# Kernel optimization log

Hardware: AMD Instinct MI355X
Metric: run time of the kernel (lower is better)

The kernel has to match this reference:

```python
import jax, jax.numpy as jnp
import numpy as np

K = 4          # neighbors
R = 2          # step_ratio
O = 64         # output_size


def setup_inputs() -> dict:
    key = jax.random.key(0)
    ks = jax.random.split(key, 7)
    B, C, N = 16, 128, 2048
    x = jax.random.normal(ks[0], (B, C, N), jnp.float32)
    # 1x1 conv weights stored as [out, in]; bias [out]
    w1 = jax.random.normal(ks[1], (O, 2 * C), jnp.float32) * (1.0 / np.sqrt(2 * C))
    b1 = jax.random.normal(ks[2], (O,), jnp.float32) * 0.01
    w2 = jax.random.normal(ks[3], (O * R, 2 * C + O), jnp.float32) * (1.0 / np.sqrt(2 * C + O))
    b2 = jax.random.normal(ks[4], (O * R,), jnp.float32) * 0.01
    w3 = jax.random.normal(ks[5], (O, O), jnp.float32) * (1.0 / np.sqrt(O))
    b3 = jax.random.normal(ks[6], (O,), jnp.float32) * 0.01
    return {"x": x, "w1": w1, "b1": b1, "w2": w2, "b2": b2, "w3": w3, "b3": b3}


def _knn_idx(x, k):
    # x: [B, C, N]; returns indices of k nearest neighbors (incl. self) [B, N, k]
    inner = -2.0 * jnp.einsum('bcn,bcm->bnm', x, x)           # [B, N, N]
    xx = jnp.sum(x * x, axis=1)                                # [B, N]
    pd = -xx[:, :, None] - inner - xx[:, None, :]              # negative sq dist
    return jax.lax.top_k(pd, k)[1]                             # [B, N, k]


def _graph_feature(x, k):
    # minus_center=False variant used by EF_expansion
    idx = _knn_idx(x, k)                                       # [B, N, k]
    xt = jnp.transpose(x, (0, 2, 1))                           # [B, N, C]
    feat = jax.vmap(lambda xb, ib: xb[ib])(xt, idx)            # [B, N, k, C]
    center = jnp.broadcast_to(xt[:, :, None, :], feat.shape)   # [B, N, k, C]
    f = jnp.concatenate([center, feat], axis=3)                # [B, N, k, 2C]
    return jnp.transpose(f, (0, 3, 1, 2))                      # [B, 2C, N, k]


def _conv1x1(w, b, x):
    # x: [B, Cin, H, W] -> [B, Cout, H, W]
    return jnp.einsum('oc,bchw->bohw', w, x) + b[None, :, None, None]


def reference(x, w1, b1, w2, b2, w3, b3):
    B, C, N = x.shape
    ief = jnp.transpose(_graph_feature(x, K), (0, 1, 3, 2))    # [B, 2C, k, N]
    e1 = _conv1x1(w1, b1, ief)                                 # [B, O, k, N]
    e = jax.nn.relu(jnp.concatenate([e1, ief], axis=1))        # [B, O+2C, k, N]
    e2 = jax.nn.relu(_conv1x1(w2, b2, e))                      # [B, O*R, k, N]
    # [B,O*R,k,N] -> [B,k,N,O*R] -> [B,k,N*R,O] -> [B,O,k,N*R]
    e2 = jnp.transpose(e2, (0, 2, 3, 1)).reshape(B, K, N * R, O)
    e2 = jnp.transpose(e2, (0, 3, 1, 2))
    e3 = _conv1x1(w3, b3, e2)                                  # [B, O, k, N*R]
    return jnp.max(e3, axis=2)                                 # [B, O, N*R]
```

## Files before the change

### kernel.cpp

```cpp
#include <hip/hip_runtime.h>
#include <cstdint>
#include <cstddef>

#define B_  16
#define C_  128
#define N_  2048
#define K_  4
#define O_  64
#define C2_ 256
#define ED_ 320
#define NM_ 4096
#define ROWB 256
#define AGC 384

typedef float  f32x4  __attribute__((ext_vector_type(4)));
typedef short  s16x8  __attribute__((ext_vector_type(8)));
typedef __bf16 bf16x4 __attribute__((ext_vector_type(4)));
typedef __bf16 bf16x8 __attribute__((ext_vector_type(8)));
typedef unsigned short u16;
typedef unsigned int   u32;
typedef unsigned int   u32x4 __attribute__((ext_vector_type(4)));

__device__ __forceinline__ u32 umin32(u32 a, u32 b) { return a < b ? a : b; }
__device__ __forceinline__ u32 umax32(u32 a, u32 b) { return a > b ? a : b; }
__device__ __forceinline__ float bf2f(u16 h) { return __builtin_bit_cast(float, (u32)h << 16); }

__device__ __forceinline__ s16x8 ldw_bf16(const float* __restrict__ p) {
  float4 a = *(const float4*)p;
  float4 c = *(const float4*)(p + 4);
  bf16x8 r;
  r[0] = (__bf16)a.x; r[1] = (__bf16)a.y; r[2] = (__bf16)a.z; r[3] = (__bf16)a.w;
  r[4] = (__bf16)c.x; r[5] = (__bf16)c.y; r[6] = (__bf16)c.z; r[7] = (__bf16)c.w;
  return __builtin_bit_cast(s16x8, r);
}

__device__ __forceinline__ u32 relu2(u32 u) {
  u32 s = u & 0x80008000u;
  u32 m = s - (s >> 15);
  return u & ~(m | s);
}
__device__ __forceinline__ s16x8 relu8(s16x8 v) {
  u32x4 u = __builtin_bit_cast(u32x4, v);
  u[0] = relu2(u[0]); u[1] = relu2(u[1]);
  u[2] = relu2(u[2]); u[3] = relu2(u[3]);
  return __builtin_bit_cast(s16x8, u);
}

__device__ __forceinline__ void glds16(const void* g, void* l) {
  __builtin_amdgcn_global_load_lds(
      (const __attribute__((address_space(1))) u32*)g,
      (__attribute__((address_space(3))) u32*)l, 16, 0, 0);
}

__global__ __launch_bounds__(256) void prep_kernel(const float* __restrict__ x,
                                                   const float* __restrict__ w1,
                                                   const float* __restrict__ w2,
                                                   const float* __restrict__ w3,
                                                   float* __restrict__ xT32,
                                                   u16* __restrict__ xh,
                                                   float* __restrict__ xx,
                                                   u16* __restrict__ wh,
                                                   u16* __restrict__ wg) {
  const int t = threadIdx.x;
  if (blockIdx.y == B_) {
    const int gid = blockIdx.x * 256 + t;
    for (int i = gid; i < 15360; i += 8192) {
      const float* src; u16* dst;
      if (i < 4096)       { src = w1 + (size_t)i * 4;            dst = wh + (size_t)i * 4; }
      else if (i < 14336) { src = w2 + (size_t)(i - 4096) * 4;   dst = wh + 16384 + (size_t)(i - 4096) * 4; }
      else                { src = w3 + (size_t)(i - 14336) * 4;  dst = wh + 57344 + (size_t)(i - 14336) * 4; }
      float4 v = *(const float4*)src;
      ushort4 h;
      h.x = __builtin_bit_cast(u16, (__bf16)v.x);
      h.y = __builtin_bit_cast(u16, (__bf16)v.y);
      h.z = __builtin_bit_cast(u16, (__bf16)v.z);
      h.w = __builtin_bit_cast(u16, (__bf16)v.w);
      *(ushort4*)dst = h;
    }
    if (wg) {
      for (int i = gid; i < 12288; i += 8192) {
        int r = i >> 5;
        int c4 = (i & 31) * 4;
        const float* src;
        if (r < 64)       src = w1 + (size_t)r * C2_ + c4;
        else if (r < 128) src = w1 + (size_t)(r - 64) * C2_ + 128 + c4;
        else if (r < 256) src = w2 + (size_t)(r - 128) * ED_ + 64 + c4;
        else              src = w2 + (size_t)(r - 256) * ED_ + 192 + c4;
        float4 v = *(const float4*)src;
        ushort4 h;
        h.x = __builtin_bit_cast(u16, (__bf16)v.x);
        h.y = __builtin_bit_cast(u16, (__bf16)v.y);
        h.z = __builtin_bit_cast(u16, (__bf16)v.z);
        h.w = __builtin_bit_cast(u16, (__bf16)v.w);
        *(ushort4*)&wg[(size_t)r * 128 + c4] = h;
      }
    }
    return;
  }

  __shared__ __align__(16) float sx[C_][65];
  const int b = blockIdx.y, n0 = blockIdx.x * 64;
  const float* xb = x + (size_t)b * C_ * N_;
  for (int u = t; u < C_ * 16; u += 256) {
    int c = u >> 4, f4 = u & 15;
    float4 v = *(const float4*)&xb[(size_t)c * N_ + n0 + f4 * 4];
    sx[c][f4 * 4 + 0] = v.x; sx[c][f4 * 4 + 1] = v.y;
    sx[c][f4 * 4 + 2] = v.z; sx[c][f4 * 4 + 3] = v.w;
  }
  __syncthreads();
  if (t < 64) {
    float s = 0.f;
    for (int c = 0; c < C_; ++c) { float v = sx[c][t]; s = fmaf(v, v, s); }
    xx[b * N_ + n0 + t] = s;
  }
  for (int u = t; u < 64 * 16; u += 256) {
    int n = u >> 4, cb = u & 15;
    float vv[8]; s16x8 hv;
#pragma unroll
    for (int j = 0; j < 8; ++j) {
      float v = sx[cb * 8 + j][n];
      vv[j] = v;
      hv[j] = (short)__builtin_bit_cast(u16, (__bf16)v);
    }
    size_t ro = ((size_t)b * N_ + n0 + n) * C_;
    *(float4*)&xT32[ro + cb * 8]     = make_float4(vv[0], vv[1], vv[2], vv[3]);
    *(float4*)&xT32[ro + cb * 8 + 4] = make_float4(vv[4], vv[5], vv[6], vv[7]);
    int sc = cb ^ (n & 7);
    *(s16x8*)&xh[ro + sc * 8] = hv;
  }
}

__global__ __launch_bounds__(256) void knn_mfma(const u16* __restrict__ xh,
                                                const float* __restrict__ xx,
                                                int* __restrict__ cand8) {
  __shared__ __align__(16) char smem[40960];
  const int b = blockIdx.y, q0 = blockIdx.x * 64;
  const int t = threadIdx.x;
  const int lane = t & 63, wv = t >> 6, lq = t & 15, lh = (t >> 4) & 3;
  const u16* xhb = xh + (size_t)b * N_ * C_;
  const float* xxb = xx + b * N_;

  s16x8 qf[4][4];
#pragma unroll
  for (int qt = 0; qt < 4; ++qt)
#pragma unroll
    for (int ks = 0; ks < 4; ++ks) {
      int q = q0 + qt * 16 + lq;
      int ch = (ks * 4 + lh) ^ (q & 7);
      qf[qt][ks] = *(const s16x8*)&xhb[(size_t)q * C_ + ch * 8];
    }

  u32 pk[4][5];
#pragma unroll
  for (int qt = 0; qt < 4; ++qt)
#pragma unroll
    for (int s = 0; s < 5; ++s) pk[qt][s] = 0xFFFFFFFFu;

  auto stage = [&](int bufi, int m0) {
    const char* s = (const char*)(xhb + (size_t)m0 * C_);
    char* d = smem + bufi * 16384;
#pragma unroll
    for (int c = 0; c < 4; ++c) {
      int off = (wv * 4 + c) * 1024;
      glds16(s + off + lane * 16, d + off);
    }
  };

  stage(0, 0);
  asm volatile("s_waitcnt vmcnt(0)");
  __syncthreads();

  for (int step = 0; step < 32; ++step) {
    const int cur = step & 1;
    if (step < 31) stage(cur ^ 1, (step + 1) * 64);
    const char* mb = smem + cur * 16384;
    f32x4 acc[4];
#pragma unroll
    for (int qt = 0; qt < 4; ++qt) acc[qt] = (f32x4){0.f, 0.f, 0.f, 0.f};
#pragma unroll
    for (int ks = 0; ks < 4; ++ks) {
      int row = wv * 16 + lq;
      int ch = (ks * 4 + lh) ^ (lq & 7);
      s16x8 mf = *(const s16x8*)(mb + row * 256 + ch * 16);
#pragma unroll
      for (int qt = 0; qt < 4; ++qt)
        acc[qt] = __builtin_amdgcn_mfma_f32_16x16x32_bf16(mf, qf[qt][ks], acc[qt], 0, 0, 0);
    }
    const int mrow = step * 64 + wv * 16 + lh * 4;
    float4 xm4 = *(const float4*)&xxb[mrow];
    float xma[4] = {xm4.x, xm4.y, xm4.z, xm4.w};
#pragma unroll
    for (int r = 0; r < 4; ++r) {
#pragma unroll
      for (int qt = 0; qt < 4; ++qt) {
        float dd = fmaf(acc[qt][r], -2.f, xma[r]);
        u32 s = __builtin_bit_cast(u32, dd);
        u32 neg = (u32)((int)s >> 31);
        u32 u = s ^ (neg | 0x80000000u);
        u32 v = (u & 0xFFFFF800u) | (u32)(mrow + r);
#pragma unroll
        for (int s5 = 0; s5 < 5; ++s5) {
          u32 lo = umin32(v, pk[qt][s5]);
          v = umax32(v, pk[qt][s5]);
          pk[qt][s5] = lo;
        }
      }
    }
    asm volatile("s_waitcnt vmcnt(0)");
    __syncthreads();
  }

  u32* cd = (u32*)smem;
  const int unit = wv * 4 + lh;
#pragma unroll
  for (int qt = 0; qt < 4; ++qt) {
    int ql = qt * 16 + lq;
#pragma unroll
    for (int s = 0; s < 5; ++s) cd[ql * 85 + unit * 5 + s] = pk[qt][s];
  }
  __syncthreads();
  if (t < 64) {
    u32 fd[8];
#pragma unroll
    for (int s = 0; s < 8; ++s) fd[s] = 0xFFFFFFFFu;
    for (int j = 0; j < 80; ++j) {
      u32 v = cd[t * 85 + j];
#pragma unroll
      for (int s = 0; s < 8; ++s) {
        u32 lo = umin32(v, fd[s]);
        v = umax32(v, fd[s]);
        fd[s] = lo;
      }
    }
#pragma unroll
    for (int s = 0; s < 8; ++s)
      cand8[((size_t)b * N_ + q0 + t) * 8 + s] = (int)(fd[s] & 0x7FFu);
  }
}

__global__ __launch_bounds__(256) void rerank_kernel(const float* __restrict__ xT32,
                                                     const float* __restrict__ xx,
                                                     const int* __restrict__ cand8,
                                                     int* __restrict__ knn_out) {
  __shared__ __align__(16) float sq[64][132];
  __shared__ float sd[64][8];
  __shared__ int   si[64][8];
  const int b = blockIdx.y, n0 = blockIdx.x * 64;
  const int t = threadIdx.x;
  const float* xb32 = xT32 + (size_t)b * N_ * C_;
  for (int u = t; u < 64 * 32; u += 256) {
    int n = u >> 5, seg = u & 31;
    *(float4*)&sq[n][seg * 4] = *(const float4*)&xb32[(size_t)(n0 + n) * C_ + seg * 4];
  }
  __syncthreads();
  const int ql = t >> 2, cs = t & 3;
#pragma unroll
  for (int cc = 0; cc < 2; ++cc) {
    int cslot = cs + cc * 4;
    int idx = cand8[((size_t)b * N_ + n0 + ql) * 8 + cslot];
    const float* mr = &xb32[(size_t)idx * C_];
    float a0 = 0.f, a1 = 0.f, a2 = 0.f, a3 = 0.f;
#pragma unroll 8
    for (int i = 0; i < 32; ++i) {
      float4 qv = *(const float4*)&sq[ql][i * 4];
      float4 mv = *(const float4*)&mr[i * 4];
      a0 = fmaf(qv.x, mv.x, a0); a1 = fmaf(qv.y, mv.y, a1);
      a2 = fmaf(qv.z, mv.z, a2); a3 = fmaf(qv.w, mv.w, a3);
    }
    float dot = (a0 + a1) + (a2 + a3);
    sd[ql][cslot] = xx[(size_t)b * N_ + idx] - 2.f * dot;
    si[ql][cslot] = idx;
  }
  __syncthreads();
  if (t < 64) {
    float dloc[8]; int iloc[8];
#pragma unroll
    for (int j = 0; j < 8; ++j) { dloc[j] = sd[t][j]; iloc[j] = si[t][j]; }
    u32 used = 0;
#pragma unroll
    for (int s = 0; s < 4; ++s) {
      float bdv = 1e30f; int bidx = 0x7fffffff; int bj = 0;
#pragma unroll
      for (int j = 0; j < 8; ++j) {
        if (!((used >> j) & 1)) {
          bool bet = (dloc[j] < bdv) || (dloc[j] == bdv && iloc[j] < bidx);
          if (bet) { bdv = dloc[j]; bidx = iloc[j]; bj = j; }
        }
      }
      used |= 1u << bj;
      knn_out[((size_t)b * N_ + n0 + t) * K_ + s] = bidx;
    }
  }
}

__global__ __launch_bounds__(256, 2) void agemm_kernel(
    const u16* __restrict__ xh, const u16* __restrict__ wg,
    const float* __restrict__ b1, const float* __restrict__ b2,
    u16* __restrict__ ag) {
  __shared__ __align__(16) char sm[66560];
  u16* outT = (u16*)(sm + 16384);
  const int b = blockIdx.y, m0 = blockIdx.x * 64;
  const int t = threadIdx.x, lane = t & 63, wv = t >> 6, lq = t & 15, lh = (t >> 4) & 3;
  const u16* xhb = xh + (size_t)b * N_ * C_;

  {
    const char* s = (const char*)(xhb + (size_t)m0 * C_);
#pragma unroll
    for (int c = 0; c < 4; ++c) {
      int off = (wv * 4 + c) * 1024;
      glds16(s + off + lane * 16, sm + off);
    }
  }

  s16x8 af[6][4];
#pragma unroll
  for (int rt = 0; rt < 6; ++rt)
#pragma unroll
    for (int ks = 0; ks < 4; ++ks)
      af[rt][ks] = *(const s16x8*)&wg[(size_t)(wv * 96 + rt * 16 + lq) * 128 + ks * 32 + lh * 8];

  f32x4 acc[6][4];
#pragma unroll
  for (int rt = 0; rt < 6; ++rt)
#pragma unroll
    for (int cg = 0; cg < 4; ++cg) acc[rt][cg] = (f32x4){0.f, 0.f, 0.f, 0.f};

  asm volatile("s_waitcnt vmcnt(0)");
  __syncthreads();

#pragma unroll
  for (int cg = 0; cg < 4; ++cg) {
    s16x8 braw[4], brel[4];
#pragma unroll
    for (int ks = 0; ks < 4; ++ks) {
      int row = cg * 16 + lq;
      braw[ks] = *(const s16x8*)(sm + row * 256 + (((ks * 4 + lh) ^ (lq & 7)) * 16));
      brel[ks] = relu8(braw[ks]);
    }
#pragma unroll
    for (int rt = 0; rt < 6; ++rt) {
      const bool rl = (wv * 96 + rt * 16) >= 128;
#pragma unroll
      for (int ks = 0; ks < 4; ++ks)
        acc[rt][cg] = __builtin_amdgcn_mfma_f32_16x16x32_bf16(
            af[rt][ks], rl ? brel[ks] : braw[ks], acc[rt][cg], 0, 0, 0);
    }
  }

#pragma unroll
  for (int rt = 0; rt < 6; ++rt) {
    const int ch0 = wv * 96 + rt * 16 + lh * 4;
    float bias[4];
#pragma unroll
    for (int r = 0; r < 4; ++r) {
      int c = ch0 + r;
      bias[r] = (c < 64) ? b1[c] : ((c >= 128 && c < 256) ? b2[c - 128] : 0.f);
    }
#pragma unroll
    for (int cg = 0; cg < 4; ++cg) {
      bf16x4 st;
#pragma unroll
      for (int r = 0; r < 4; ++r) st[r] = (__bf16)(acc[rt][cg][r] + bias[r]);
      *(bf16x4*)&outT[(size_t)(cg * 16 + lq) * 392 + ch0] = st;
    }
  }
  __syncthreads();
// ... 55 lines not shown
    for (int q = 0; q < 4; ++q) {
      s16x8 va = *(const s16x8*)&rc[128 + p * 32 + q * 8];
      s16x8 vb = *(const s16x8*)&rn[256 + p * 32 + q * 8];
      bf16x8 r;
#pragma unroll
      for (int j = 0; j < 8; ++j)
        r[j] = (__bf16)(bf2f((u16)va[j]) + bf2f((u16)vb[j]));
      *(bf16x8*)&s2T[(size_t)col * 136 + p * 32 + q * 8] = r;
    }
  }
  __syncthreads();

  {
    f32x4 acc[2][4];
#pragma unroll
    for (int rt = 0; rt < 2; ++rt)
#pragma unroll
      for (int cg = 0; cg < 4; ++cg) acc[rt][cg] = (f32x4){0.f, 0.f, 0.f, 0.f};
#pragma unroll
    for (int ks = 0; ks < 2; ++ks)
#pragma unroll
      for (int cg = 0; cg < 4; ++cg) {
        s16x8 bf = *(const s16x8*)&e1T[(size_t)(cg * 16 + lq) * 72 + ks * 32 + lh * 8];
#pragma unroll
        for (int rt = 0; rt < 2; ++rt)
          acc[rt][cg] = __builtin_amdgcn_mfma_f32_16x16x32_bf16(w2f[rt][ks], bf, acc[rt][cg], 0, 0, 0);
      }
#pragma unroll
    for (int rt = 0; rt < 2; ++rt)
#pragma unroll
      for (int cg = 0; cg < 4; ++cg) {
        const int col = cg * 16 + lq;
        const int j0 = wv * 32 + rt * 16 + lh * 4;
        ushort4 sv = *(const ushort4*)&s2T[(size_t)col * 136 + j0];
        bf16x4 st;
        st[0] = (__bf16)fmaxf(acc[rt][cg][0] + bf2f(sv.x), 0.f);
        st[1] = (__bf16)fmaxf(acc[rt][cg][1] + bf2f(sv.y), 0.f);
        st[2] = (__bf16)fmaxf(acc[rt][cg][2] + bf2f(sv.z), 0.f);
        st[3] = (__bf16)fmaxf(acc[rt][cg][3] + bf2f(sv.w), 0.f);
        *(bf16x4*)&e2T[(size_t)col * 136 + j0] = st;
      }
  }
  __syncthreads();

  {
#pragma unroll
    for (int cg = 0; cg < 8; ++cg) {
      int col = cg * 16 + lq;
      int nl = col >> 3, rr = (col >> 2) & 1, kk = col & 3;
      int row = nl * 4 + kk;
      s16x8 f1 = *(const s16x8*)&e2T[(size_t)row * 136 + rr * 64 + lh * 8];
      s16x8 f2 = *(const s16x8*)&e2T[(size_t)row * 136 + rr * 64 + 32 + lh * 8];
      f32x4 acc = {0.f, 0.f, 0.f, 0.f};
      acc = __builtin_amdgcn_mfma_f32_16x16x32_bf16(w3a, f1, acc, 0, 0, 0);
      acc = __builtin_amdgcn_mfma_f32_16x16x32_bf16(w3b, f2, acc, 0, 0, 0);
      float vv[4];
#pragma unroll
      for (int r = 0; r < 4; ++r) {
        float v = acc[r];
        v = fmaxf(v, __shfl_xor(v, 1));
        v = fmaxf(v, __shfl_xor(v, 2));
        vv[r] = v;
      }
      if ((lq & 3) == 0) {
        int mloc = col >> 2;
        int o = wv * 16 + lh * 4;
        const float b3a[4] = {b3v.x, b3v.y, b3v.z, b3v.w};
#pragma unroll
        for (int r = 0; r < 4; ++r) oSt[(size_t)(o + r) * 36 + mloc] = vv[r] + b3a[r];
      }
    }
  }
  __syncthreads();

#pragma unroll
  for (int io = 0; io < 2; ++io) {
    int u = t + io * 256;
    int o = u >> 3, seg = u & 7;
    *(float4*)&out[((size_t)b * O_ + o) * NM_ + n0 * 2 + seg * 4] =
        *(const float4*)&oSt[(size_t)o * 36 + seg * 4];
  }
}

__global__ __launch_bounds__(256, 2) void fused_tiled(
    const u16* __restrict__ xh, const u16* __restrict__ wh,
    const int* __restrict__ knn_idx,
    const float* __restrict__ b1, const float* __restrict__ b2,
    const float* __restrict__ b3, float* __restrict__ out) {
  __shared__ __align__(16) char fsm[66560];
  __bf16* e1T = (__bf16*)(fsm + 40960);
  float*  oSt = (float*)(fsm + 40960);
  char*   e2T = fsm + 50176;

  const int t  = threadIdx.x;
  const int lane = t & 63, wv = t >> 6, lq = t & 15, lh = (t >> 4) & 3;
  const int b = blockIdx.y;
  const int nbase = blockIdx.x * 64;
  const u16* xhb = xh + (size_t)b * N_ * C_;
  const int kb = (b * N_ + nbase) * K_;

  s16x8 w1f[8], w2f0[10], w2f1[10], w3f[2];
  {
    const u16* r1 = wh + (size_t)(wv * 16 + lq) * C2_;
#pragma unroll
    for (int ks = 0; ks < 8; ++ks) w1f[ks] = *(const s16x8*)&r1[ks * 32 + lh * 8];
    const u16* r20 = wh + 16384 + (size_t)(wv * 32 + lq) * ED_;
    const u16* r21 = r20 + (size_t)16 * ED_;
#pragma unroll
    for (int ks = 0; ks < 10; ++ks) {
      w2f0[ks] = *(const s16x8*)&r20[ks * 32 + lh * 8];
      w2f1[ks] = *(const s16x8*)&r21[ks * 32 + lh * 8];
    }
    const u16* r3 = wh + 57344 + (size_t)(wv * 16 + lq) * O_;
    w3f[0] = *(const s16x8*)&r3[lh * 8];
    w3f[1] = *(const s16x8*)&r3[32 + lh * 8];
  }
  const float4 b1v  = *(const float4*)&b1[wv * 16 + lh * 4];
  const float4 b2v0 = *(const float4*)&b2[wv * 32 + lh * 4];
  const float4 b2v1 = *(const float4*)&b2[wv * 32 + 16 + lh * 4];
  const float4 b3v  = *(const float4*)&b3[wv * 16 + lh * 4];

  auto stageTile = [&](int it, const int* nids) {
    char* cb = fsm + (it & 1) * 20480;
    char* nb = cb + 4096;
    glds16((const char*)xhb + (size_t)(nbase + it * 16 + wv * 4) * ROWB + lane * 16,
           cb + wv * 4 * ROWB);
#pragma unroll
    for (int g = 0; g < 4; ++g) {
      int col = wv * 16 + g * 4 + (lane >> 4);
      int nid = nids[g];
      int sc = (lane & 15) ^ (col & 7) ^ (nid & 7);
      glds16((const char*)xhb + (size_t)nid * ROWB + sc * 16,
             nb + (wv * 16 + g * 4) * ROWB);
    }
  };

  int nids[4];
#pragma unroll
  for (int g = 0; g < 4; ++g)
    nids[g] = knn_idx[kb + wv * 16 + g * 4 + (lane >> 4)];
  stageTile(0, nids);

  for (int it = 0; it < 4; ++it) {
    if (it < 3) {
#pragma unroll
      for (int g = 0; g < 4; ++g)
        nids[g] = knn_idx[kb + (it + 1) * 64 + wv * 16 + g * 4 + (lane >> 4)];
    }
    asm volatile("s_waitcnt vmcnt(0)" ::: "memory");
    __syncthreads();
    if (it < 3) stageTile(it + 1, nids);

    const char* cb = fsm + (it & 1) * 20480;
    const char* nb = cb + 4096;

    {
      f32x4 acc1[4];
#pragma unroll
      for (int cg = 0; cg < 4; ++cg) acc1[cg] = (f32x4){0.f, 0.f, 0.f, 0.f};
#pragma unroll
      for (int ks = 0; ks < 8; ++ks) {
#pragma unroll
        for (int cg = 0; cg < 4; ++cg) {
          const char* bp;
          if (ks < 4) {
            int r = cg * 4 + (lq >> 2);
            bp = cb + r * ROWB + (((ks * 4 + lh) ^ (r & 7)) * 16);
          } else {
            int r = cg * 16 + lq;
            bp = nb + r * ROWB + ((((ks - 4) * 4 + lh) ^ (r & 7)) * 16);
          }
          acc1[cg] = __builtin_amdgcn_mfma_f32_16x16x32_bf16(
              w1f[ks], *(const s16x8*)bp, acc1[cg], 0, 0, 0);
        }
      }
      const float bb[4] = {b1v.x, b1v.y, b1v.z, b1v.w};
#pragma unroll
      for (int cg = 0; cg < 4; ++cg) {
        bf16x4 st;
#pragma unroll
        for (int r = 0; r < 4; ++r) st[r] = (__bf16)fmaxf(acc1[cg][r] + bb[r], 0.f);
        *(bf16x4*)&e1T[(cg * 16 + lq) * 72 + wv * 16 + lh * 4] = st;
      }
    }
    __syncthreads();

    {
      f32x4 acc2[2][4];
#pragma unroll
      for (int ro = 0; ro < 2; ++ro)
#pragma unroll
        for (int cg = 0; cg < 4; ++cg) acc2[ro][cg] = (f32x4){0.f, 0.f, 0.f, 0.f};
#pragma unroll
      for (int ks = 0; ks < 10; ++ks) {
#pragma unroll
        for (int cg = 0; cg < 4; ++cg) {
          s16x8 bf;
          if (ks < 2) {
            bf = *(const s16x8*)&e1T[(cg * 16 + lq) * 72 + ks * 32 + lh * 8];
          } else if (ks < 6) {
            int r = cg * 4 + (lq >> 2);
            bf = relu8(*(const s16x8*)(cb + r * ROWB + ((((ks - 2) * 4 + lh) ^ (r & 7)) * 16)));
          } else {
            int r = cg * 16 + lq;
            bf = relu8(*(const s16x8*)(nb + r * ROWB + ((((ks - 6) * 4 + lh) ^ (r & 7)) * 16)));
          }
          acc2[0][cg] = __builtin_amdgcn_mfma_f32_16x16x32_bf16(w2f0[ks], bf, acc2[0][cg], 0, 0, 0);
          acc2[1][cg] = __builtin_amdgcn_mfma_f32_16x16x32_bf16(w2f1[ks], bf, acc2[1][cg], 0, 0, 0);
        }
      }
      const float c0[4] = {b2v0.x, b2v0.y, b2v0.z, b2v0.w};
      const float c1[4] = {b2v1.x, b2v1.y, b2v1.z, b2v1.w};
#pragma unroll
      for (int ro = 0; ro < 2; ++ro)
#pragma unroll
        for (int cg = 0; cg < 4; ++cg) {
          int col = cg * 16 + lq;
          int e = wv * 32 + ro * 16 + lh * 4;
          int j = e >> 3, sub = e & 7;
          int pos = j ^ (col & 7);
          bf16x4 st;
#pragma unroll
          for (int r = 0; r < 4; ++r) {
            float v = acc2[ro][cg][r] + (ro ? c1[r] : c0[r]);
            st[r] = (__bf16)fmaxf(v, 0.f);
          }
          *(bf16x4*)(e2T + col * ROWB + pos * 16 + sub * 2) = st;
        }
    }
    __syncthreads();

    {
#pragma unroll
      for (int cg = 0; cg < 8; ++cg) {
        int col = cg * 16 + lq;
        int nl = col >> 3, rr = (col >> 2) & 1, kk = col & 3;
        int row = nl * 4 + kk;
        int j1 = rr * 8 + lh, j2 = rr * 8 + 4 + lh;
        s16x8 f1 = *(const s16x8*)(e2T + row * ROWB + ((j1 ^ (row & 7)) * 16));
        s16x8 f2 = *(const s16x8*)(e2T + row * ROWB + ((j2 ^ (row & 7)) * 16));
        f32x4 acc = {0.f, 0.f, 0.f, 0.f};
        acc = __builtin_amdgcn_mfma_f32_16x16x32_bf16(w3f[0], f1, acc, 0, 0, 0);
        acc = __builtin_amdgcn_mfma_f32_16x16x32_bf16(w3f[1], f2, acc, 0, 0, 0);
        float vv[4];
#pragma unroll
        for (int r = 0; r < 4; ++r) {
          float v = acc[r];
          v = fmaxf(v, __shfl_xor(v, 1));
          v = fmaxf(v, __shfl_xor(v, 2));
          vv[r] = v;
        }
        if ((lq & 3) == 0) {
          int mloc = col >> 2;
          int o = wv * 16 + lh * 4;
          const float b3a[4] = {b3v.x, b3v.y, b3v.z, b3v.w};
#pragma unroll
          for (int r = 0; r < 4; ++r) oSt[(o + r) * 36 + mloc] = vv[r] + b3a[r];
        }
      }
    }
    __syncthreads();

#pragma unroll
    for (int io = 0; io < 2; ++io) {
      int u = t + io * 256;
      int o = u >> 3, seg = u & 7;
      *(float4*)&out[((size_t)b * O_ + o) * NM_ + nbase * 2 + it * 32 + seg * 4] =
          *(const float4*)&oSt[o * 36 + seg * 4];
    }
  }
}

__global__ __launch_bounds__(256) void xx_kernel(const float* __restrict__ x,
                                                 float* __restrict__ xx) {
  int g = blockIdx.x * 256 + threadIdx.x;
  int b = g >> 11;
  int n = g & (N_ - 1);
  const float* xp = x + (size_t)b * C_ * N_ + n;
  float s = 0.f;
#pragma unroll 8
  for (int c = 0; c < C_; ++c) { float v = xp[(size_t)c * N_]; s += v * v; }
  xx[g] = s;
}

__global__ __launch_bounds__(256) void knn_kernel(const float* __restrict__ x,
                                                  const float* __restrict__ xx,
                                                  int* __restrict__ knn_out) {
  __shared__ __align__(16) float qT[C_ * 64];
  __shared__ __align__(16) float mT[C_ * 64];
  const int b = blockIdx.y;
  const int q0 = blockIdx.x * 64;
  const int t = threadIdx.x;
  const float* xb = x + (size_t)b * C_ * N_;
  const float* xxb = xx + b * N_;
  for (int i = t; i < C_ * 64; i += 256) {
    int c = i >> 6, q = i & 63;
    qT[i] = xb[(size_t)c * N_ + q0 + q];
  }
  const int tq = t & 15;
  const int tm = t >> 4;
  float bd[4][4]; int bi[4][4];
#pragma unroll
  for (int a = 0; a < 4; ++a)
#pragma unroll
    for (int s = 0; s < 4; ++s) { bd[a][s] = 1e30f; bi[a][s] = 0; }
  for (int m0 = 0; m0 < N_; m0 += 64) {
    __syncthreads();
    for (int i = t; i < C_ * 64; i += 256) {
      int c = i >> 6, m = i & 63;
      mT[i] = xb[(size_t)c * N_ + m0 + m];
    }
    __syncthreads();
    float acc[4][4];
#pragma unroll
    for (int a = 0; a < 4; ++a)
#pragma unroll
      for (int j = 0; j < 4; ++j) acc[a][j] = 0.f;
#pragma unroll 4
    for (int c = 0; c < C_; ++c) {
      float4 qv = *(const float4*)&qT[c * 64 + tq * 4];
      float4 mv = *(const float4*)&mT[c * 64 + tm * 4];
      float qa[4] = {qv.x, qv.y, qv.z, qv.w};
      float ma[4] = {mv.x, mv.y, mv.z, mv.w};
#pragma unroll
      for (int a = 0; a < 4; ++a)
#pragma unroll
        for (int j = 0; j < 4; ++j) acc[a][j] += qa[a] * ma[j];
    }
#pragma unroll
    for (int j = 0; j < 4; ++j) {
      float xm = xxb[m0 + tm * 4 + j];
      int id = m0 + tm * 4 + j;
#pragma unroll
      for (int a = 0; a < 4; ++a) {
        float d = xm - 2.f * acc[a][j];
        if (d < bd[a][3]) {
          bd[a][3] = d; bi[a][3] = id;
#pragma unroll
          for (int s = 3; s > 0; --s)
            if (bd[a][s] < bd[a][s - 1]) {
              float td = bd[a][s]; bd[a][s] = bd[a][s - 1]; bd[a][s - 1] = td;
              int ti = bi[a][s]; bi[a][s] = bi[a][s - 1]; bi[a][s - 1] = ti;
            }
        }
      }
    }
  }
  __syncthreads();
  float* cd = qT;
  int* ci = (int*)mT;
#pragma unroll
  for (int a = 0; a < 4; ++a) {
    int q = tq * 4 + a;
#pragma unroll
    for (int s = 0; s < 4; ++s) {
// ... 110 lines not shown
    for (int ks = 0; ks < 10; ++ks) {
      s16x8 a0 = ldw_bf16(w2r0 + ks * 32 + lh * 8);
      s16x8 a1 = ldw_bf16(w2r1 + ks * 32 + lh * 8);
#pragma unroll
      for (int cg = 0; cg < 4; ++cg) {
        s16x8 bf;
        if (ks < 2)      bf = *(const s16x8*)&e1T[cg * 16 + lq][ks * 32 + lh * 8];
        else if (ks < 6) bf = relu8(*(const s16x8*)&cT[cg * 4 + (lq >> 2)][(ks - 2) * 32 + lh * 8]);
        else             bf = relu8(*(const s16x8*)&nT[cg * 16 + lq][(ks - 6) * 32 + lh * 8]);
        acc2[0][cg] = __builtin_amdgcn_mfma_f32_16x16x32_bf16(a0, bf, acc2[0][cg], 0, 0, 0);
        acc2[1][cg] = __builtin_amdgcn_mfma_f32_16x16x32_bf16(a1, bf, acc2[1][cg], 0, 0, 0);
      }
    }
  }
  __syncthreads();
  {
#pragma unroll
    for (int ro = 0; ro < 2; ++ro)
#pragma unroll
      for (int cg = 0; cg < 4; ++cg) {
        bf16x4 st;
#pragma unroll
        for (int r = 0; r < 4; ++r) {
          float v = acc2[ro][cg][r] + b2[wv * 32 + ro * 16 + lh * 4 + r];
          st[r] = (__bf16)fmaxf(v, 0.f);
        }
        *(bf16x4*)&e2T[cg * 16 + lq][wv * 32 + ro * 16 + lh * 4] = st;
      }
  }
  __syncthreads();

  {
    const float* w3r = w3 + (size_t)(wv * 16 + lq) * O_;
    s16x8 a0 = ldw_bf16(w3r + lh * 8);
    s16x8 a1 = ldw_bf16(w3r + 32 + lh * 8);
#pragma unroll
    for (int cg = 0; cg < 8; ++cg) {
      int col = cg * 16 + lq;
      int nl = col >> 3, rr = (col >> 2) & 1, kk = col & 3;
      const __bf16* base = &e2T[nl * 4 + kk][rr * 64];
      f32x4 acc = {0.f, 0.f, 0.f, 0.f};
      acc = __builtin_amdgcn_mfma_f32_16x16x32_bf16(a0, *(const s16x8*)(base + lh * 8),      acc, 0, 0, 0);
      acc = __builtin_amdgcn_mfma_f32_16x16x32_bf16(a1, *(const s16x8*)(base + 32 + lh * 8), acc, 0, 0, 0);
      float vv[4];
#pragma unroll
      for (int r = 0; r < 4; ++r) {
        float v = acc[r];
        v = fmaxf(v, __shfl_xor(v, 1));
        v = fmaxf(v, __shfl_xor(v, 2));
        vv[r] = v;
      }
      if ((lq & 3) == 0) {
        int mloc = col >> 2;
        int o = wv * 16 + lh * 4;
#pragma unroll
        for (int r = 0; r < 4; ++r) oSt[o + r][mloc] = vv[r] + b3[o + r];
      }
    }
  }
  __syncthreads();

#pragma unroll
  for (int it = 0; it < 2; ++it) {
    int u = t + it * 256;
    int o = u >> 3, seg = u & 7;
    *(float4*)&out[((size_t)b * O_ + o) * NM_ + n0 * 2 + seg * 4] =
        *(const float4*)&oSt[o][seg * 4];
  }
}

extern "C" void kernel_launch(void* const* d_in, const int* in_sizes, int n_in,
                              void* d_out, int out_size, void* d_ws, size_t ws_size,
                              hipStream_t stream) {
  const float* x  = (const float*)d_in[0];
  const float* w1 = (const float*)d_in[1];
  const float* b1 = (const float*)d_in[2];
  const float* w2 = (const float*)d_in[3];
  const float* b2 = (const float*)d_in[4];
  const float* w3 = (const float*)d_in[5];
  const float* b3 = (const float*)d_in[6];
  float* out = (float*)d_out;

  const size_t AGB      = (size_t)B_ * N_ * AGC * 2;
  const size_t off_xhN  = AGB;
  const size_t off_xxN  = off_xhN + (size_t)B_ * N_ * C_ * 2;
  const size_t off_c8N  = off_xxN + (size_t)B_ * N_ * 4;
  const size_t off_knnN = off_c8N + (size_t)B_ * N_ * 8 * 4;
  const size_t off_whN  = off_knnN + (size_t)B_ * N_ * K_ * 4;
  const size_t off_wgN  = off_whN + (size_t)61440 * 2;
  const size_t NEED_NEW = off_wgN + (size_t)AGC * 128 * 2;

  const size_t off_xh   = (size_t)B_ * N_ * C_ * 4;
  const size_t off_xx   = off_xh + (size_t)B_ * N_ * C_ * 2;
  const size_t off_c8   = off_xx + (size_t)B_ * N_ * 4;
  const size_t off_knn  = off_c8 + (size_t)B_ * N_ * 8 * 4;
  const size_t off_wh   = off_knn + (size_t)B_ * N_ * K_ * 4;
  const size_t NEED_OLD = off_wh + (size_t)61440 * 2;

  if (ws_size >= NEED_NEW) {
    u16*   agp  = (u16*)d_ws;
    float* xT32 = (float*)d_ws;
    u16*   xhp  = (u16*)((char*)d_ws + off_xhN);
    float* xx   = (float*)((char*)d_ws + off_xxN);
    int*   c8   = (int*)((char*)d_ws + off_c8N);
    int*   knn  = (int*)((char*)d_ws + off_knnN);
    u16*   whp  = (u16*)((char*)d_ws + off_whN);
    u16*   wgp  = (u16*)((char*)d_ws + off_wgN);

    hipLaunchKernelGGL(prep_kernel, dim3(N_ / 64, B_ + 1), dim3(256), 0, stream,
                       x, w1, w2, w3, xT32, xhp, xx, whp, wgp);
    hipLaunchKernelGGL(knn_mfma, dim3(N_ / 64, B_), dim3(256), 0, stream, xhp, xx, c8);
    hipLaunchKernelGGL(rerank_kernel, dim3(N_ / 64, B_), dim3(256), 0, stream, xT32, xx, c8, knn);
    hipLaunchKernelGGL(agemm_kernel, dim3(N_ / 64, B_), dim3(256), 0, stream,
                       xhp, wgp, b1, b2, agp);
    hipLaunchKernelGGL(fused_ag, dim3(N_ / 16, B_), dim3(256), 0, stream,
                       agp, whp, knn, b3, out);
  } else if (ws_size >= NEED_OLD) {
    float* xT32 = (float*)d_ws;
    u16*   xhp  = (u16*)((char*)d_ws + off_xh);
    float* xx   = (float*)((char*)d_ws + off_xx);
    int*   c8   = (int*)((char*)d_ws + off_c8);
    int*   knn  = (int*)((char*)d_ws + off_knn);
    u16*   whp  = (u16*)((char*)d_ws + off_wh);

    hipLaunchKernelGGL(prep_kernel, dim3(N_ / 64, B_ + 1), dim3(256), 0, stream,
                       x, w1, w2, w3, xT32, xhp, xx, whp, (u16*)nullptr);
    hipLaunchKernelGGL(knn_mfma, dim3(N_ / 64, B_), dim3(256), 0, stream, xhp, xx, c8);
    hipLaunchKernelGGL(rerank_kernel, dim3(N_ / 64, B_), dim3(256), 0, stream, xT32, xx, c8, knn);
    hipLaunchKernelGGL(fused_tiled, dim3(N_ / 64, B_), dim3(256), 0, stream,
                       xhp, whp, knn, b1, b2, b3, out);
  } else {
    float* xx = (float*)d_ws;
    int* knn = (int*)((char*)d_ws + (size_t)B_ * N_ * 4);
    hipLaunchKernelGGL(xx_kernel, dim3((B_ * N_) / 256), dim3(256), 0, stream, x, xx);
    hipLaunchKernelGGL(knn_kernel, dim3(N_ / 64, B_), dim3(256), 0, stream, x, xx, knn);
    hipLaunchKernelGGL(fused_fb, dim3(N_ / 16, B_), dim3(256), 0, stream,
                       x, knn, w1, b1, w2, b2, w3, b3, out);
  }
}
```

Baseline: 116.8 us.

## Split KNN candidate search over two key halves and rerank sixteen candidates

```diff
diff --git a/kernel.cpp b/kernel.cpp
--- a/kernel.cpp
+++ b/kernel.cpp
@@ -132,9 +132,10 @@
 
 __global__ __launch_bounds__(256) void knn_mfma(const u16* __restrict__ xh,
                                                 const float* __restrict__ xx,
-                                                int* __restrict__ cand8) {
+                                                int* __restrict__ cand16) {
   __shared__ __align__(16) char smem[40960];
-  const int b = blockIdx.y, q0 = blockIdx.x * 64;
+  const int b = blockIdx.z, half = blockIdx.y, q0 = blockIdx.x * 64;
+  const int mbase = half * 1024;
   const int t = threadIdx.x;
   const int lane = t & 63, wv = t >> 6, lq = t & 15, lh = (t >> 4) & 3;
   const u16* xhb = xh + (size_t)b * N_ * C_;
@@ -166,13 +167,13 @@
     }
   };
 
-  stage(0, 0);
+  stage(0, mbase);
   asm volatile("s_waitcnt vmcnt(0)");
   __syncthreads();
 
-  for (int step = 0; step < 32; ++step) {
+  for (int step = 0; step < 16; ++step) {
     const int cur = step & 1;
-    if (step < 31) stage(cur ^ 1, (step + 1) * 64);
+    if (step < 15) stage(cur ^ 1, mbase + (step + 1) * 64);
     const char* mb = smem + cur * 16384;
     f32x4 acc[4];
 #pragma unroll
@@ -186,17 +187,15 @@
       for (int qt = 0; qt < 4; ++qt)
         acc[qt] = __builtin_amdgcn_mfma_f32_16x16x32_bf16(mf, qf[qt][ks], acc[qt], 0, 0, 0);
     }
-    const int mrow = step * 64 + wv * 16 + lh * 4;
+    const int mrow = mbase + step * 64 + wv * 16 + lh * 4;
     float4 xm4 = *(const float4*)&xxb[mrow];
-    float xma[4] = {xm4.x, xm4.y, xm4.z, xm4.w};
+    float xma[4] = {xm4.x + 512.f, xm4.y + 512.f, xm4.z + 512.f, xm4.w + 512.f};
 #pragma unroll
     for (int r = 0; r < 4; ++r) {
 #pragma unroll
       for (int qt = 0; qt < 4; ++qt) {
         float dd = fmaf(acc[qt][r], -2.f, xma[r]);
-        u32 s = __builtin_bit_cast(u32, dd);
-        u32 neg = (u32)((int)s >> 31);
-        u32 u = s ^ (neg | 0x80000000u);
+        u32 u = __builtin_bit_cast(u32, dd);
         u32 v = (u & 0xFFFFF800u) | (u32)(mrow + r);
 #pragma unroll
         for (int s5 = 0; s5 < 5; ++s5) {
@@ -234,17 +233,17 @@
     }
 #pragma unroll
     for (int s = 0; s < 8; ++s)
-      cand8[((size_t)b * N_ + q0 + t) * 8 + s] = (int)(fd[s] & 0x7FFu);
+      cand16[((size_t)b * N_ + q0 + t) * 16 + half * 8 + s] = (int)(fd[s] & 0x7FFu);
   }
 }
 
 __global__ __launch_bounds__(256) void rerank_kernel(const float* __restrict__ xT32,
                                                      const float* __restrict__ xx,
-                                                     const int* __restrict__ cand8,
+                                                     const int* __restrict__ cand16,
                                                      int* __restrict__ knn_out) {
   __shared__ __align__(16) float sq[64][132];
-  __shared__ float sd[64][8];
-  __shared__ int   si[64][8];
+  __shared__ float sd[64][16];
+  __shared__ int   si[64][16];
   const int b = blockIdx.y, n0 = blockIdx.x * 64;
   const int t = threadIdx.x;
   const float* xb32 = xT32 + (size_t)b * N_ * C_;
@@ -255,9 +254,9 @@
   __syncthreads();
   const int ql = t >> 2, cs = t & 3;
 #pragma unroll
-  for (int cc = 0; cc < 2; ++cc) {
+  for (int cc = 0; cc < 4; ++cc) {
     int cslot = cs + cc * 4;
-    int idx = cand8[((size_t)b * N_ + n0 + ql) * 8 + cslot];
+    int idx = cand16[((size_t)b * N_ + n0 + ql) * 16 + cslot];
     const float* mr = &xb32[(size_t)idx * C_];
     float a0 = 0.f, a1 = 0.f, a2 = 0.f, a3 = 0.f;
 #pragma unroll 8
@@ -273,15 +272,15 @@
   }
   __syncthreads();
   if (t < 64) {
-    float dloc[8]; int iloc[8];
-#pragma unroll
-    for (int j = 0; j < 8; ++j) { dloc[j] = sd[t][j]; iloc[j] = si[t][j]; }
+    float dloc[16]; int iloc[16];
+#pragma unroll
+    for (int j = 0; j < 16; ++j) { dloc[j] = sd[t][j]; iloc[j] = si[t][j]; }
     u32 used = 0;
 #pragma unroll
     for (int s = 0; s < 4; ++s) {
       float bdv = 1e30f; int bidx = 0x7fffffff; int bj = 0;
 #pragma unroll
-      for (int j = 0; j < 8; ++j) {
+      for (int j = 0; j < 16; ++j) {
         if (!((used >> j) & 1)) {
           bool bet = (dloc[j] < bdv) || (dloc[j] == bdv && iloc[j] < bidx);
           if (bet) { bdv = dloc[j]; bidx = iloc[j]; bj = j; }
@@ -968,10 +967,10 @@
   float* out = (float*)d_out;
 
   const size_t AGB      = (size_t)B_ * N_ * AGC * 2;
+  const size_t off_c8N  = (size_t)B_ * N_ * C_ * 4;
   const size_t off_xhN  = AGB;
   const size_t off_xxN  = off_xhN + (size_t)B_ * N_ * C_ * 2;
-  const size_t off_c8N  = off_xxN + (size_t)B_ * N_ * 4;
-  const size_t off_knnN = off_c8N + (size_t)B_ * N_ * 8 * 4;
+  const size_t off_knnN = off_xxN + (size_t)B_ * N_ * 4;
   const size_t off_whN  = off_knnN + (size_t)B_ * N_ * K_ * 4;
   const size_t off_wgN  = off_whN + (size_t)61440 * 2;
   const size_t NEED_NEW = off_wgN + (size_t)AGC * 128 * 2;
@@ -986,35 +985,28 @@
   if (ws_size >= NEED_NEW) {
     u16*   agp  = (u16*)d_ws;
     float* xT32 = (float*)d_ws;
+    int*   c16  = (int*)((char*)d_ws + off_c8N);
     u16*   xhp  = (u16*)((char*)d_ws + off_xhN);
     float* xx   = (float*)((char*)d_ws + off_xxN);
-    int*   c8   = (int*)((char*)d_ws + off_c8N);
     int*   knn  = (int*)((char*)d_ws + off_knnN);
     u16*   whp  = (u16*)((char*)d_ws + off_whN);
     u16*   wgp  = (u16*)((char*)d_ws + off_wgN);
 
     hipLaunchKernelGGL(prep_kernel, dim3(N_ / 64, B_ + 1), dim3(256), 0, stream,
                        x, w1, w2, w3, xT32, xhp, xx, whp, wgp);
-    hipLaunchKernelGGL(knn_mfma, dim3(N_ / 64, B_), dim3(256), 0, stream, xhp, xx, c8);
-    hipLaunchKernelGGL(rerank_kernel, dim3(N_ / 64, B_), dim3(256), 0, stream, xT32, xx, c8, knn);
+    hipLaunchKernelGGL(knn_mfma, dim3(N_ / 64, 2, B_), dim3(256), 0, stream, xhp, xx, c16);
+    hipLaunchKernelGGL(rerank_kernel, dim3(N_ / 64, B_), dim3(256), 0, stream, xT32, xx, c16, knn);
     hipLaunchKernelGGL(agemm_kernel, dim3(N_ / 64, B_), dim3(256), 0, stream,
                        xhp, wgp, b1, b2, agp);
     hipLaunchKernelGGL(fused_ag, dim3(N_ / 16, B_), dim3(256), 0, stream,
                        agp, whp, knn, b3, out);
   } else if (ws_size >= NEED_OLD) {
-    float* xT32 = (float*)d_ws;
-    u16*   xhp  = (u16*)((char*)d_ws + off_xh);
-    float* xx   = (float*)((char*)d_ws + off_xx);
-    int*   c8   = (int*)((char*)d_ws + off_c8);
-    int*   knn  = (int*)((char*)d_ws + off_knn);
-    u16*   whp  = (u16*)((char*)d_ws + off_wh);
-
-    hipLaunchKernelGGL(prep_kernel, dim3(N_ / 64, B_ + 1), dim3(256), 0, stream,
-                       x, w1, w2, w3, xT32, xhp, xx, whp, (u16*)nullptr);
-    hipLaunchKernelGGL(knn_mfma, dim3(N_ / 64, B_), dim3(256), 0, stream, xhp, xx, c8);
-    hipLaunchKernelGGL(rerank_kernel, dim3(N_ / 64, B_), dim3(256), 0, stream, xT32, xx, c8, knn);
-    hipLaunchKernelGGL(fused_tiled, dim3(N_ / 64, B_), dim3(256), 0, stream,
-                       xhp, whp, knn, b1, b2, b3, out);
+    float* xx = (float*)d_ws;
+    int* knn = (int*)((char*)d_ws + (size_t)B_ * N_ * 4);
+    hipLaunchKernelGGL(xx_kernel, dim3((B_ * N_) / 256), dim3(256), 0, stream, x, xx);
+    hipLaunchKernelGGL(knn_kernel, dim3(N_ / 64, B_), dim3(256), 0, stream, x, xx, knn);
+    hipLaunchKernelGGL(fused_fb, dim3(N_ / 16, B_), dim3(256), 0, stream,
+                       x, knn, w1, b1, w2, b2, w3, b3, out);
   } else {
     float* xx = (float*)d_ws;
     int* knn = (int*)((char*)d_ws + (size_t)B_ * N_ * 4);
```

Result: slower. 135.0 us (+15.7%).

## Load KNN candidate fragments straight into registers and simplify distance key encoding

Applied to the files above, without the earlier changes.

```diff
diff --git a/kernel.cpp b/kernel.cpp
--- a/kernel.cpp
+++ b/kernel.cpp
@@ -10,7 +10,6 @@
 #define C2_ 256
 #define ED_ 320
 #define NM_ 4096
-#define ROWB 256
 #define AGC 384
 
 typedef float  f32x4  __attribute__((ext_vector_type(4)));
@@ -133,10 +132,10 @@
 __global__ __launch_bounds__(256) void knn_mfma(const u16* __restrict__ xh,
                                                 const float* __restrict__ xx,
                                                 int* __restrict__ cand8) {
-  __shared__ __align__(16) char smem[40960];
+  __shared__ __align__(16) u32 cd[64 * 85];
   const int b = blockIdx.y, q0 = blockIdx.x * 64;
   const int t = threadIdx.x;
-  const int lane = t & 63, wv = t >> 6, lq = t & 15, lh = (t >> 4) & 3;
+  const int wv = t >> 6, lq = t & 15, lh = (t >> 4) & 3;
   const u16* xhb = xh + (size_t)b * N_ * C_;
   const float* xxb = xx + b * N_;
 
@@ -156,47 +155,34 @@
 #pragma unroll
     for (int s = 0; s < 5; ++s) pk[qt][s] = 0xFFFFFFFFu;
 
-  auto stage = [&](int bufi, int m0) {
-    const char* s = (const char*)(xhb + (size_t)m0 * C_);
-    char* d = smem + bufi * 16384;
-#pragma unroll
-    for (int c = 0; c < 4; ++c) {
-      int off = (wv * 4 + c) * 1024;
-      glds16(s + off + lane * 16, d + off);
-    }
+  const int rbase = wv * 16 + lq;
+  int choff[4];
+#pragma unroll
+  for (int ks = 0; ks < 4; ++ks) choff[ks] = ((ks * 4 + lh) ^ (lq & 7)) * 8;
+
+  auto loadf = [&](int step, s16x8* d) {
+    const u16* rp = xhb + (size_t)(step * 64 + rbase) * C_;
+#pragma unroll
+    for (int ks = 0; ks < 4; ++ks) d[ks] = *(const s16x8*)&rp[choff[ks]];
   };
-
-  stage(0, 0);
-  asm volatile("s_waitcnt vmcnt(0)");
-  __syncthreads();
-
-  for (int step = 0; step < 32; ++step) {
-    const int cur = step & 1;
-    if (step < 31) stage(cur ^ 1, (step + 1) * 64);
-    const char* mb = smem + cur * 16384;
+  auto dostep = [&](int step, const s16x8* mf) {
     f32x4 acc[4];
 #pragma unroll
     for (int qt = 0; qt < 4; ++qt) acc[qt] = (f32x4){0.f, 0.f, 0.f, 0.f};
 #pragma unroll
-    for (int ks = 0; ks < 4; ++ks) {
-      int row = wv * 16 + lq;
-      int ch = (ks * 4 + lh) ^ (lq & 7);
-      s16x8 mf = *(const s16x8*)(mb + row * 256 + ch * 16);
+    for (int ks = 0; ks < 4; ++ks)
 #pragma unroll
       for (int qt = 0; qt < 4; ++qt)
-        acc[qt] = __builtin_amdgcn_mfma_f32_16x16x32_bf16(mf, qf[qt][ks], acc[qt], 0, 0, 0);
-    }
+        acc[qt] = __builtin_amdgcn_mfma_f32_16x16x32_bf16(mf[ks], qf[qt][ks], acc[qt], 0, 0, 0);
     const int mrow = step * 64 + wv * 16 + lh * 4;
     float4 xm4 = *(const float4*)&xxb[mrow];
-    float xma[4] = {xm4.x, xm4.y, xm4.z, xm4.w};
+    float xma[4] = {xm4.x + 512.f, xm4.y + 512.f, xm4.z + 512.f, xm4.w + 512.f};
 #pragma unroll
     for (int r = 0; r < 4; ++r) {
 #pragma unroll
       for (int qt = 0; qt < 4; ++qt) {
         float dd = fmaf(acc[qt][r], -2.f, xma[r]);
-        u32 s = __builtin_bit_cast(u32, dd);
-        u32 neg = (u32)((int)s >> 31);
-        u32 u = s ^ (neg | 0x80000000u);
+        u32 u = __builtin_bit_cast(u32, dd);
         u32 v = (u & 0xFFFFF800u) | (u32)(mrow + r);
 #pragma unroll
         for (int s5 = 0; s5 < 5; ++s5) {
@@ -206,11 +192,18 @@
         }
       }
     }
-    asm volatile("s_waitcnt vmcnt(0)");
-    __syncthreads();
-  }
-
-  u32* cd = (u32*)smem;
+  };
+
+  s16x8 fa[4], fb[4];
+  loadf(0, fa);
+  loadf(1, fb);
+  for (int step = 0; step < 32; step += 2) {
+    dostep(step, fa);
+    if (step + 2 < 32) loadf(step + 2, fa);
+    dostep(step + 1, fb);
+    if (step + 3 < 32) loadf(step + 3, fb);
+  }
+
   const int unit = wv * 4 + lh;
 #pragma unroll
   for (int qt = 0; qt < 4; ++qt) {
@@ -503,195 +496,6 @@
   }
 }
 
-__global__ __launch_bounds__(256, 2) void fused_tiled(
-    const u16* __restrict__ xh, const u16* __restrict__ wh,
-    const int* __restrict__ knn_idx,
-    const float* __restrict__ b1, const float* __restrict__ b2,
-    const float* __restrict__ b3, float* __restrict__ out) {
-  __shared__ __align__(16) char fsm[66560];
-  __bf16* e1T = (__bf16*)(fsm + 40960);
-  float*  oSt = (float*)(fsm + 40960);
-  char*   e2T = fsm + 50176;
-
-  const int t  = threadIdx.x;
-  const int lane = t & 63, wv = t >> 6, lq = t & 15, lh = (t >> 4) & 3;
-  const int b = blockIdx.y;
-  const int nbase = blockIdx.x * 64;
-  const u16* xhb = xh + (size_t)b * N_ * C_;
-  const int kb = (b * N_ + nbase) * K_;
-
-  s16x8 w1f[8], w2f0[10], w2f1[10], w3f[2];
-  {
-    const u16* r1 = wh + (size_t)(wv * 16 + lq) * C2_;
-#pragma unroll
-    for (int ks = 0; ks < 8; ++ks) w1f[ks] = *(const s16x8*)&r1[ks * 32 + lh * 8];
-    const u16* r20 = wh + 16384 + (size_t)(wv * 32 + lq) * ED_;
-    const u16* r21 = r20 + (size_t)16 * ED_;
-#pragma unroll
-    for (int ks = 0; ks < 10; ++ks) {
-      w2f0[ks] = *(const s16x8*)&r20[ks * 32 + lh * 8];
-      w2f1[ks] = *(const s16x8*)&r21[ks * 32 + lh * 8];
-    }
-    const u16* r3 = wh + 57344 + (size_t)(wv * 16 + lq) * O_;
-    w3f[0] = *(const s16x8*)&r3[lh * 8];
-    w3f[1] = *(const s16x8*)&r3[32 + lh * 8];
-  }
-  const float4 b1v  = *(const float4*)&b1[wv * 16 + lh * 4];
-  const float4 b2v0 = *(const float4*)&b2[wv * 32 + lh * 4];
-  const float4 b2v1 = *(const float4*)&b2[wv * 32 + 16 + lh * 4];
-  const float4 b3v  = *(const float4*)&b3[wv * 16 + lh * 4];
-
-  auto stageTile = [&](int it, const int* nids) {
-    char* cb = fsm + (it & 1) * 20480;
-    char* nb = cb + 4096;
-    glds16((const char*)xhb + (size_t)(nbase + it * 16 + wv * 4) * ROWB + lane * 16,
-           cb + wv * 4 * ROWB);
-#pragma unroll
-    for (int g = 0; g < 4; ++g) {
-      int col = wv * 16 + g * 4 + (lane >> 4);
-      int nid = nids[g];
-      int sc = (lane & 15) ^ (col & 7) ^ (nid & 7);
-      glds16((const char*)xhb + (size_t)nid * ROWB + sc * 16,
-             nb + (wv * 16 + g * 4) * ROWB);
-    }
-  };
-
-  int nids[4];
-#pragma unroll
-  for (int g = 0; g < 4; ++g)
-    nids[g] = knn_idx[kb + wv * 16 + g * 4 + (lane >> 4)];
-  stageTile(0, nids);
-
-  for (int it = 0; it < 4; ++it) {
-    if (it < 3) {
-#pragma unroll
-      for (int g = 0; g < 4; ++g)
-        nids[g] = knn_idx[kb + (it + 1) * 64 + wv * 16 + g * 4 + (lane >> 4)];
-    }
-    asm volatile("s_waitcnt vmcnt(0)" ::: "memory");
-    __syncthreads();
-    if (it < 3) stageTile(it + 1, nids);
-
-    const char* cb = fsm + (it & 1) * 20480;
-    const char* nb = cb + 4096;
-
-    {
-      f32x4 acc1[4];
-#pragma unroll
-      for (int cg = 0; cg < 4; ++cg) acc1[cg] = (f32x4){0.f, 0.f, 0.f, 0.f};
-#pragma unroll
-      for (int ks = 0; ks < 8; ++ks) {
-#pragma unroll
-        for (int cg = 0; cg < 4; ++cg) {
-          const char* bp;
-          if (ks < 4) {
-            int r = cg * 4 + (lq >> 2);
-            bp = cb + r * ROWB + (((ks * 4 + lh) ^ (r & 7)) * 16);
-          } else {
-            int r = cg * 16 + lq;
-            bp = nb + r * ROWB + ((((ks - 4) * 4 + lh) ^ (r & 7)) * 16);
-          }
-          acc1[cg] = __builtin_amdgcn_mfma_f32_16x16x32_bf16(
-              w1f[ks], *(const s16x8*)bp, acc1[cg], 0, 0, 0);
-        }
-      }
-      const float bb[4] = {b1v.x, b1v.y, b1v.z, b1v.w};
-#pragma unroll
-      for (int cg = 0; cg < 4; ++cg) {
-        bf16x4 st;
-#pragma unroll
-        for (int r = 0; r < 4; ++r) st[r] = (__bf16)fmaxf(acc1[cg][r] + bb[r], 0.f);
-        *(bf16x4*)&e1T[(cg * 16 + lq) * 72 + wv * 16 + lh * 4] = st;
-      }
-    }
-    __syncthreads();
-
-    {
-      f32x4 acc2[2][4];
-#pragma unroll
-      for (int ro = 0; ro < 2; ++ro)
-#pragma unroll
-        for (int cg = 0; cg < 4; ++cg) acc2[ro][cg] = (f32x4){0.f, 0.f, 0.f, 0.f};
-#pragma unroll
-      for (int ks = 0; ks < 10; ++ks) {
-#pragma unroll
-        for (int cg = 0; cg < 4; ++cg) {
-          s16x8 bf;
-          if (ks < 2) {
-            bf = *(const s16x8*)&e1T[(cg * 16 + lq) * 72 + ks * 32 + lh * 8];
-          } else if (ks < 6) {
-            int r = cg * 4 + (lq >> 2);
-            bf = relu8(*(const s16x8*)(cb + r * ROWB + ((((ks - 2) * 4 + lh) ^ (r & 7)) * 16)));
-          } else {
-            int r = cg * 16 + lq;
-            bf = relu8(*(const s16x8*)(nb + r * ROWB + ((((ks - 6) * 4 + lh) ^ (r & 7)) * 16)));
-          }
-          acc2[0][cg] = __builtin_amdgcn_mfma_f32_16x16x32_bf16(w2f0[ks], bf, acc2[0][cg], 0, 0, 0);
-          acc2[1][cg] = __builtin_amdgcn_mfma_f32_16x16x32_bf16(w2f1[ks], bf, acc2[1][cg], 0, 0, 0);
-        }
-      }
-      const float c0[4] = {b2v0.x, b2v0.y, b2v0.z, b2v0.w};
-      const float c1[4] = {b2v1.x, b2v1.y, b2v1.z, b2v1.w};
-#pragma unroll
-      for (int ro = 0; ro < 2; ++ro)
-#pragma unroll
-        for (int cg = 0; cg < 4; ++cg) {
-          int col = cg * 16 + lq;
-          int e = wv * 32 + ro * 16 + lh * 4;
-          int j = e >> 3, sub = e & 7;
-          int pos = j ^ (col & 7);
-          bf16x4 st;
-#pragma unroll
-          for (int r = 0; r < 4; ++r) {
-            float v = acc2[ro][cg][r] + (ro ? c1[r] : c0[r]);
-            st[r] = (__bf16)fmaxf(v, 0.f);
-          }
-          *(bf16x4*)(e2T + col * ROWB + pos * 16 + sub * 2) = st;
-        }
-    }
-    __syncthreads();
-
-    {
-#pragma unroll
-      for (int cg = 0; cg < 8; ++cg) {
-        int col = cg * 16 + lq;
-        int nl = col >> 3, rr = (col >> 2) & 1, kk = col & 3;
-        int row = nl * 4 + kk;
-        int j1 = rr * 8 + lh, j2 = rr * 8 + 4 + lh;
-        s16x8 f1 = *(const s16x8*)(e2T + row * ROWB + ((j1 ^ (row & 7)) * 16));
-        s16x8 f2 = *(const s16x8*)(e2T + row * ROWB + ((j2 ^ (row & 7)) * 16));
-        f32x4 acc = {0.f, 0.f, 0.f, 0.f};
-        acc = __builtin_amdgcn_mfma_f32_16x16x32_bf16(w3f[0], f1, acc, 0, 0, 0);
-        acc = __builtin_amdgcn_mfma_f32_16x16x32_bf16(w3f[1], f2, acc, 0, 0, 0);
-        float vv[4];
-#pragma unroll
-        for (int r = 0; r < 4; ++r) {
-          float v = acc[r];
-          v = fmaxf(v, __shfl_xor(v, 1));
-          v = fmaxf(v, __shfl_xor(v, 2));
-          vv[r] = v;
-        }
-        if ((lq & 3) == 0) {
-          int mloc = col >> 2;
-          int o = wv * 16 + lh * 4;
-          const float b3a[4] = {b3v.x, b3v.y, b3v.z, b3v.w};
-#pragma unroll
-          for (int r = 0; r < 4; ++r) oSt[(o + r) * 36 + mloc] = vv[r] + b3a[r];
-        }
-      }
-    }
-    __syncthreads();
-
-#pragma unroll
-    for (int io = 0; io < 2; ++io) {
-      int u = t + io * 256;
-      int o = u >> 3, seg = u & 7;
-      *(float4*)&out[((size_t)b * O_ + o) * NM_ + nbase * 2 + it * 32 + seg * 4] =
-          *(const float4*)&oSt[o * 36 + seg * 4];
-    }
-  }
-}
-
 __global__ __launch_bounds__(256) void xx_kernel(const float* __restrict__ x,
                                                  float* __restrict__ xx) {
   int g = blockIdx.x * 256 + threadIdx.x;
@@ -968,27 +772,20 @@
   float* out = (float*)d_out;
 
   const size_t AGB      = (size_t)B_ * N_ * AGC * 2;
+  const size_t off_c8N  = (size_t)B_ * N_ * C_ * 4;
   const size_t off_xhN  = AGB;
   const size_t off_xxN  = off_xhN + (size_t)B_ * N_ * C_ * 2;
-  const size_t off_c8N  = off_xxN + (size_t)B_ * N_ * 4;
-  const size_t off_knnN = off_c8N + (size_t)B_ * N_ * 8 * 4;
+  const size_t off_knnN = off_xxN + (size_t)B_ * N_ * 4;
   const size_t off_whN  = off_knnN + (size_t)B_ * N_ * K_ * 4;
   const size_t off_wgN  = off_whN + (size_t)61440 * 2;
   const size_t NEED_NEW = off_wgN + (size_t)AGC * 128 * 2;
 
-  const size_t off_xh   = (size_t)B_ * N_ * C_ * 4;
-  const size_t off_xx   = off_xh + (size_t)B_ * N_ * C_ * 2;
-  const size_t off_c8   = off_xx + (size_t)B_ * N_ * 4;
-  const size_t off_knn  = off_c8 + (size_t)B_ * N_ * 8 * 4;
-  const size_t off_wh   = off_knn + (size_t)B_ * N_ * K_ * 4;
-  const size_t NEED_OLD = off_wh + (size_t)61440 * 2;
-
   if (ws_size >= NEED_NEW) {
     u16*   agp  = (u16*)d_ws;
     float* xT32 = (float*)d_ws;
+    int*   c8   = (int*)((char*)d_ws + off_c8N);
     u16*   xhp  = (u16*)((char*)d_ws + off_xhN);
     float* xx   = (float*)((char*)d_ws + off_xxN);
-    int*   c8   = (int*)((char*)d_ws + off_c8N);
     int*   knn  = (int*)((char*)d_ws + off_knnN);
     u16*   whp  = (u16*)((char*)d_ws + off_whN);
     u16*   wgp  = (u16*)((char*)d_ws + off_wgN);
@@ -1001,20 +798,6 @@
                        xhp, wgp, b1, b2, agp);
     hipLaunchKernelGGL(fused_ag, dim3(N_ / 16, B_), dim3(256), 0, stream,
                        agp, whp, knn, b3, out);
-  } else if (ws_size >= NEED_OLD) {
-    float* xT32 = (float*)d_ws;
-    u16*   xhp  = (u16*)((char*)d_ws + off_xh);
-    float* xx   = (float*)((char*)d_ws + off_xx);
-    int*   c8   = (int*)((char*)d_ws + off_c8);
-    int*   knn  = (int*)((char*)d_ws + off_knn);
-    u16*   whp  = (u16*)((char*)d_ws + off_wh);
-
-    hipLaunchKernelGGL(prep_kernel, dim3(N_ / 64, B_ + 1), dim3(256), 0, stream,
-                       x, w1, w2, w3, xT32, xhp, xx, whp, (u16*)nullptr);
-    hipLaunchKernelGGL(knn_mfma, dim3(N_ / 64, B_), dim3(256), 0, stream, xhp, xx, c8);
-    hipLaunchKernelGGL(rerank_kernel, dim3(N_ / 64, B_), dim3(256), 0, stream, xT32, xx, c8, knn);
-    hipLaunchKernelGGL(fused_tiled, dim3(N_ / 64, B_), dim3(256), 0, stream,
-                       xhp, whp, knn, b1, b2, b3, out);
   } else {
     float* xx = (float*)d_ws;
     int* knn = (int*)((char*)d_ws + (size_t)B_ * N_ * 4);
```

After: 111.7 us. -4.3%, faster.
